# Performance work log

Hardware: AMD Instinct MI355X
Metric: run time of the kernel (lower is better)

## Reference

```python
import jax, jax.numpy as jnp
import numpy as np

B, S, E, H, A, D, V, L = 64, 196, 512, 512, 256, 512, 32000, 32
PAD_IDX = 2


def setup_inputs() -> dict:
    key = jax.random.key(0)
    ks = jax.random.split(key, 20)
    sc = 0.02
    return {
        "encoder_out": jax.random.normal(ks[0], (B, S, E), jnp.float32),
        "pooled": jax.random.normal(ks[1], (B, E), jnp.float32),
        "targets": jax.random.randint(ks[2], (B, L), 0, V, jnp.int64),
        "embedding": jax.random.normal(ks[3], (V, D), jnp.float32) * sc,
        "W_enc": jax.random.normal(ks[4], (A, E), jnp.float32) * sc,
        "b_enc": jnp.zeros((A,), jnp.float32),
        "W_dec": jax.random.normal(ks[5], (A, H), jnp.float32) * sc,
        "b_dec": jnp.zeros((A,), jnp.float32),
        "W_score": jax.random.normal(ks[6], (1, A), jnp.float32) * sc,
        "b_score": jnp.zeros((1,), jnp.float32),
        "W_ih": jax.random.normal(ks[7], (3 * H, D + E), jnp.float32) * sc,
        "W_hh": jax.random.normal(ks[8], (3 * H, H), jnp.float32) * sc,
        "b_ih": jnp.zeros((3 * H,), jnp.float32),
        "b_hh": jnp.zeros((3 * H,), jnp.float32),
        "W_out": jax.random.normal(ks[9], (V, H), jnp.float32) * sc,
        "b_out": jnp.zeros((V,), jnp.float32),
        "W_init": jax.random.normal(ks[10], (H, E), jnp.float32) * sc,
        "b_init": jnp.zeros((H,), jnp.float32),
    }


def reference(encoder_out, pooled, targets, embedding, W_enc, b_enc, W_dec,
              b_dec, W_score, b_score, W_ih, W_hh, b_ih, b_hh, W_out, b_out,
              W_init, b_init):
    # padding_idx=2: that embedding row is zero
    emb_tab = embedding.at[PAD_IDX].set(0.0)
    # initial hidden state from pooled features
    h0 = jnp.tanh(pooled @ W_init.T + b_init)              # (B, H)
    # encoder projection is step-invariant; hoist out of the loop
    enc_proj = jnp.einsum('bse,ae->bsa', encoder_out, W_enc) + b_enc  # (B,S,A)
    # teacher forcing (ratio=1.0): inputs are targets[:, :-1]
    tokens = targets[:, :-1].T                              # (L-1, B)

    def step(h, tok):
        embedded = emb_tab[tok]                             # (B, D)
        # Bahdanau attention
        dec_proj = h @ W_dec.T + b_dec                      # (B, A)
        energy = jnp.tanh(enc_proj + dec_proj[:, None, :])  # (B, S, A)
        scores = jnp.einsum('bsa,a->bs', energy, W_score[0]) + b_score[0]
        weights = jax.nn.softmax(scores, axis=1)            # (B, S)
        context = jnp.einsum('bs,bse->be', weights, encoder_out)  # (B, E)
        # GRU cell (PyTorch gate ordering: r, z, n)
        x = jnp.concatenate([embedded, context], axis=1)    # (B, D+E)
        gi = x @ W_ih.T + b_ih                              # (B, 3H)
        gh = h @ W_hh.T + b_hh                              # (B, 3H)
        gi_r, gi_z, gi_n = jnp.split(gi, 3, axis=1)
        gh_r, gh_z, gh_n = jnp.split(gh, 3, axis=1)
        r = jax.nn.sigmoid(gi_r + gh_r)
        z = jax.nn.sigmoid(gi_z + gh_z)
        n = jnp.tanh(gi_n + r * gh_n)
        h_new = (1.0 - z) * n + z * h
        logits = h_new @ W_out.T + b_out                    # (B, V)
        return h_new, logits

    _, logits = jax.lax.scan(step, h0, tokens)              # (L-1, B, V)
    return jnp.transpose(logits, (1, 0, 2))                 # (B, L-1, V)
```

## Files before the change

### kernel.cpp

```cpp
#include <hip/hip_runtime.h>

using bf16x8 = __attribute__((ext_vector_type(8))) short;
using f32x4  = __attribute__((ext_vector_type(4))) float;

__device__ inline float bf2f(unsigned short h){
  union { unsigned int u; float f; } v; v.u = ((unsigned int)h) << 16; return v.f;
}
__device__ inline unsigned short f2b(float x){
  union { float f; unsigned int u; } v; v.f = x;
  unsigned int r = (v.u + 0x7FFFu + ((v.u >> 16) & 1u)) >> 16;
  return (unsigned short)r;
}

__global__ void conv_k(const float* __restrict__ s, unsigned short* __restrict__ d, int n){
  int i = (blockIdx.x * 256 + threadIdx.x) * 4;
  if (i >= n) return;
  float4 v = *(const float4*)(s + i);
  unsigned int p0 = (unsigned int)f2b(v.x) | ((unsigned int)f2b(v.y) << 16);
  unsigned int p1 = (unsigned int)f2b(v.z) | ((unsigned int)f2b(v.w) << 16);
  *(uint2*)(d + i) = make_uint2(p0, p1);
}

__global__ void embed_k(const int* __restrict__ tgt, const float* __restrict__ emb,
                        unsigned short* __restrict__ out, int n){
  int idx = blockIdx.x * 256 + threadIdx.x;
  if (idx >= n) return;
  int d = idx & 511, m = idx >> 9, t = m >> 6, b = m & 63;
  int tok = tgt[b * 32 + t];
  float v = (tok == 2) ? 0.f : emb[(long)tok * 512 + d];
  out[idx] = f2b(v);
}

#define EPI_PLAIN 0
#define EPI_TANH  1
#define EPI_OUT   2

template<int EPI, bool AF32>
__global__ __launch_bounds__(256)
void gemm_bt(const void* __restrict__ Av, int lda,
             const unsigned short* __restrict__ Bp, int ldb,
             const float* __restrict__ bias,
             float* __restrict__ Cf, unsigned short* __restrict__ Cb, int ldc,
             int K,
             int n_split, const void* __restrict__ A2v,
             const unsigned short* __restrict__ B2p, int lda2, int ldb2)
{
  __shared__ __align__(16) unsigned short As[64][40];
  __shared__ __align__(16) unsigned short Bs[256][40];

  int m0 = blockIdx.x * 64;
  int n0 = blockIdx.y * 256;
  const void* Ap = Av; const unsigned short* Bq = Bp;
  int la = lda, lb = ldb, nB = n0;
  if (n_split > 0 && n0 >= n_split){ Ap = A2v; Bq = B2p; la = lda2; lb = ldb2; nB = n0 - n_split; }

  int tid  = threadIdx.x;
  int wave = tid >> 6, lane = tid & 63, quad = lane >> 4, lrow = lane & 15;

  f32x4 acc[4][4];
#pragma unroll
  for (int i = 0; i < 4; ++i)
#pragma unroll
    for (int j = 0; j < 4; ++j)
#pragma unroll
      for (int r = 0; r < 4; ++r) acc[i][j][r] = 0.f;

  int ar = tid >> 2, ac = (tid & 3) * 8;

  for (int k0 = 0; k0 < K; k0 += 32){
    if (AF32){
      const float* A32 = (const float*)Ap;
      const float4* src = (const float4*)(A32 + (long)(m0 + ar) * la + k0 + ac);
      float4 x0 = src[0], x1 = src[1];
      unsigned int p0 = (unsigned int)f2b(x0.x) | ((unsigned int)f2b(x0.y) << 16);
      unsigned int p1 = (unsigned int)f2b(x0.z) | ((unsigned int)f2b(x0.w) << 16);
      unsigned int p2 = (unsigned int)f2b(x1.x) | ((unsigned int)f2b(x1.y) << 16);
      unsigned int p3 = (unsigned int)f2b(x1.z) | ((unsigned int)f2b(x1.w) << 16);
      *(uint4*)&As[ar][ac] = make_uint4(p0, p1, p2, p3);
    } else {
      const unsigned short* A16 = (const unsigned short*)Ap;
      *(uint4*)&As[ar][ac] = *(const uint4*)(A16 + (long)(m0 + ar) * la + k0 + ac);
    }
#pragma unroll
    for (int c = 0; c < 4; ++c){
      int id = tid + c * 256; int br = id >> 2, bc = (id & 3) * 8;
      *(uint4*)&Bs[br][bc] = *(const uint4*)(Bq + (long)(nB + br) * lb + k0 + bc);
    }
    __syncthreads();

    bf16x8 af[4], bfr[4];
#pragma unroll
    for (int mf = 0; mf < 4; ++mf) af[mf]  = *(const bf16x8*)&As[mf * 16 + lrow][quad * 8];
#pragma unroll
    for (int nf = 0; nf < 4; ++nf) bfr[nf] = *(const bf16x8*)&Bs[wave * 64 + nf * 16 + lrow][quad * 8];
#pragma unroll
    for (int mf = 0; mf < 4; ++mf)
#pragma unroll
      for (int nf = 0; nf < 4; ++nf)
        acc[mf][nf] = __builtin_amdgcn_mfma_f32_16x16x32_bf16(af[mf], bfr[nf], acc[mf][nf], 0, 0, 0);
    __syncthreads();
  }

#pragma unroll
  for (int mf = 0; mf < 4; ++mf){
#pragma unroll
    for (int nf = 0; nf < 4; ++nf){
#pragma unroll
      for (int r = 0; r < 4; ++r){
        int m = m0 + mf * 16 + quad * 4 + r;
        int n = n0 + wave * 64 + nf * 16 + lrow;
        float v = acc[mf][nf][r];
        if (bias) v += bias[n];
        if (EPI == EPI_TANH){
          v = tanhf(v);
          Cf[(long)m * ldc + n] = v;
          Cb[(long)m * ldc + n] = f2b(v);
        } else if (EPI == EPI_OUT){
          Cf[(long)(m & 63) * (31 * 32000) + (long)(m >> 6) * 32000 + n] = v;
        } else {
          Cf[(long)m * ldc + n] = v;
        }
      }
    }
  }
}

__global__ __launch_bounds__(512)
void attn_step(const float* __restrict__ enc_proj,
               const float* __restrict__ enc_out,
               const float* __restrict__ W_score,
               const float* __restrict__ b_dec,
               const float* __restrict__ b_hh,
               const float* __restrict__ gi_emb,
               const float* __restrict__ giq,
               float* __restrict__ h_all,
               unsigned short* __restrict__ h_b16,
               const unsigned short* __restrict__ Wdec,
               unsigned short* __restrict__ ctx_b16,
               int t, int do_gates, int do_attn)
{
  int b = blockIdx.x, tid = threadIdx.x;
  __shared__ float sh_h[512];
  __shared__ float sdp[256];
  __shared__ float sbuf[512];
  __shared__ float sw[256];
  __shared__ float sred[512];
  __shared__ float swsc[256];

  float hv;
  if (do_gates){
    int j = tid;
    long ge = ((long)(t - 1) * 64 + b) * 1536;
    long gq = (long)b * 3072;
    float gir = gi_emb[ge + j]        + giq[gq + j];
    float giz = gi_emb[ge + 512 + j]  + giq[gq + 512 + j];
    float gin = gi_emb[ge + 1024 + j] + giq[gq + 1024 + j];
    float ghr = giq[gq + 1536 + j]        + b_hh[j];
    float ghz = giq[gq + 1536 + 512 + j]  + b_hh[512 + j];
    float ghn = giq[gq + 1536 + 1024 + j] + b_hh[1024 + j];
    float rr = 1.f / (1.f + __expf(-(gir + ghr)));
    float zz = 1.f / (1.f + __expf(-(giz + ghz)));
    float nn = tanhf(gin + rr * ghn);
    float hp = h_all[((long)(t - 1) * 64 + b) * 512 + j];
    hv = (1.f - zz) * nn + zz * hp;
    h_all[((long)t * 64 + b) * 512 + j] = hv;
    h_b16[((long)t * 64 + b) * 512 + j] = f2b(hv);
  } else {
    hv = h_all[((long)t * 64 + b) * 512 + tid];
  }
  sh_h[tid] = hv;
  if (tid < 256) swsc[tid] = W_score[tid];
  __syncthreads();
  if (!do_attn) return;

  {
    int a = tid & 255, half = tid >> 8;
    const uint4* wp = (const uint4*)(Wdec + a * 512 + half * 256);
    const float* hp = &sh_h[half * 256];
    float acc = 0.f;
#pragma unroll 8
    for (int c = 0; c < 32; ++c){
      uint4 wv = wp[c];
      acc += hp[c*8+0] * bf2f((unsigned short)(wv.x & 0xffff));
      acc += hp[c*8+1] * bf2f((unsigned short)(wv.x >> 16));
      acc += hp[c*8+2] * bf2f((unsigned short)(wv.y & 0xffff));
      acc += hp[c*8+3] * bf2f((unsigned short)(wv.y >> 16));
      acc += hp[c*8+4] * bf2f((unsigned short)(wv.z & 0xffff));
      acc += hp[c*8+5] * bf2f((unsigned short)(wv.z >> 16));
      acc += hp[c*8+6] * bf2f((unsigned short)(wv.w & 0xffff));
      acc += hp[c*8+7] * bf2f((unsigned short)(wv.w >> 16));
    }
    sbuf[tid] = acc;
    __syncthreads();
    if (tid < 256) sdp[tid] = sbuf[tid] + sbuf[tid + 256] + b_dec[tid];
    __syncthreads();
  }

  {
    int s = tid & 255, half = tid >> 8;
    float acc = 0.f;
    if (s < 196){
      const float* ep = enc_proj + ((long)b * 196 + s) * 256 + half * 128;
      const float* dp = &sdp[half * 128];
      const float* wv = &swsc[half * 128];
#pragma unroll 4
      for (int a = 0; a < 128; ++a){
        float x = ep[a] + dp[a];
        float e = __expf(2.f * x);
        acc += wv[a] * (1.f - 2.f / (e + 1.f));
      }
    }
    sbuf[tid] = acc;
    __syncthreads();
    float sc = (tid < 196) ? (sbuf[tid] + sbuf[tid + 256]) : -1e30f;
    sred[tid] = sc; __syncthreads();
    for (int off = 256; off > 0; off >>= 1){
      if (tid < off) sred[tid] = fmaxf(sred[tid], sred[tid + off]);
      __syncthreads();
    }
    float mx = sred[0]; __syncthreads();
    float e = (tid < 196) ? __expf(sc - mx) : 0.f;
    sred[tid] = e; __syncthreads();
    for (int off = 256; off > 0; off >>= 1){
      if (tid < off) sred[tid] += sred[tid + off];
      __syncthreads();
    }
    float inv = 1.f / sred[0];
    if (tid < 196) sw[tid] = e * inv;
    __syncthreads();
  }

  {
    const float* ep = enc_out + (long)b * 196 * 512 + tid;
    float acc = 0.f;
#pragma unroll 4
    for (int s = 0; s < 196; ++s) acc += sw[s] * ep[(long)s * 512];
    ctx_b16[b * 512 + tid] = f2b(acc);
  }
}

extern "C" void kernel_launch(void* const* d_in, const int* in_sizes, int n_in,
                              void* d_out, int out_size, void* d_ws, size_t ws_size,
                              hipStream_t stream)
{
  (void)in_sizes; (void)n_in; (void)out_size; (void)ws_size;
  const float* encoder_out = (const float*)d_in[0];
  const float* pooled      = (const float*)d_in[1];
  const int*   targets     = (const int*)d_in[2];
  const float* embedding   = (const float*)d_in[3];
  const float* W_enc  = (const float*)d_in[4];
  const float* b_enc  = (const float*)d_in[5];
  const float* W_dec  = (const float*)d_in[6];
  const float* b_dec  = (const float*)d_in[7];
  const float* W_score= (const float*)d_in[8];
  const float* W_ih   = (const float*)d_in[10];
  const float* W_hh   = (const float*)d_in[11];
  const float* b_ih   = (const float*)d_in[12];
  const float* b_hh   = (const float*)d_in[13];
  const float* W_out  = (const float*)d_in[14];
  const float* b_out  = (const float*)d_in[15];
  const float* W_init = (const float*)d_in[16];
  const float* b_init = (const float*)d_in[17];
  float* out = (float*)d_out;

  char* w = (char*)d_ws;
  float* enc_proj         = (float*)w;          w += 12845056;
  float* gi_emb           = (float*)w;          w += 12189696;
  float* h_all            = (float*)w;          w += 4194304;
  unsigned short* h_b16   = (unsigned short*)w; w += 2097152;
  float* giq              = (float*)w;          w += 786432;
  unsigned short* ctx_b16 = (unsigned short*)w; w += 65536;
  unsigned short* emb_b16 = (unsigned short*)w; w += 2031616;
  unsigned short* Wout_b  = (unsigned short*)w; w += 32768000;
  unsigned short* Wih_b   = (unsigned short*)w; w += 3145728;
  unsigned short* Whh_b   = (unsigned short*)w; w += 1572864;
  unsigned short* Wdec_b  = (unsigned short*)w; w += 262144;
  unsigned short* Winit_b = (unsigned short*)w; w += 524288;
  unsigned short* Wenc_b  = (unsigned short*)w; w += 262144;

  auto conv = [&](const float* s, unsigned short* d, int n){
    conv_k<<<dim3((n / 4 + 255) / 256), dim3(256), 0, stream>>>(s, d, n);
  };
  conv(W_out,  Wout_b,  32000 * 512);
  conv(W_ih,   Wih_b,   1536 * 1024);
  conv(W_hh,   Whh_b,   1536 * 512);
  conv(W_dec,  Wdec_b,  256 * 512);
  conv(W_init, Winit_b, 512 * 512);
  conv(W_enc,  Wenc_b,  256 * 512);
  embed_k<<<dim3((1984 * 512) / 256), dim3(256), 0, stream>>>(targets, embedding, emb_b16, 1984 * 512);

  gemm_bt<EPI_TANH, true><<<dim3(1, 2), 256, 0, stream>>>(
      pooled, 512, Winit_b, 512, b_init, h_all, h_b16, 512, 512, 0, nullptr, nullptr, 0, 0);
  gemm_bt<EPI_PLAIN, true><<<dim3(196, 1), 256, 0, stream>>>(
      encoder_out, 512, Wenc_b, 512, b_enc, enc_proj, nullptr, 256, 512, 0, nullptr, nullptr, 0, 0);
  gemm_bt<EPI_PLAIN, false><<<dim3(31, 6), 256, 0, stream>>>(
      emb_b16, 512, Wih_b, 1024, b_ih, gi_emb, nullptr, 1536, 512, 0, nullptr, nullptr, 0, 0);

  for (int t = 0; t < 31; ++t){
    attn_step<<<dim3(64), dim3(512), 0, stream>>>(
        enc_proj, encoder_out, W_score, b_dec, b_hh, gi_emb, giq,
        h_all, h_b16, Wdec_b, ctx_b16, t, (t > 0) ? 1 : 0, 1);
    gemm_bt<EPI_PLAIN, false><<<dim3(1, 12), 256, 0, stream>>>(
        ctx_b16, 512, Wih_b + 512, 1024, nullptr, giq, nullptr, 3072, 512,
        1536, h_b16 + (long)t * 64 * 512, Whh_b, 512, 512);
  }
  attn_step<<<dim3(64), dim3(512), 0, stream>>>(
      enc_proj, encoder_out, W_score, b_dec, b_hh, gi_emb, giq,
      h_all, h_b16, Wdec_b, ctx_b16, 31, 1, 0);

  gemm_bt<EPI_OUT, false><<<dim3(31, 125), 256, 0, stream>>>(
      h_b16 + 64 * 512, 512, Wout_b, 512, b_out, out, nullptr, 0, 512,
      0, nullptr, nullptr, 0, 0);
}
```

Before: 2.380 ms.

## Fuse whole recurrent decode loop into one persistent per-batch kernel

Replaces the 31-step loop of attention kernel plus gate GEMM launches with a single kernel. Each of 64 blocks (1024 threads) runs all timesteps for one batch row, keeping h, context and gate pre-activations in shared memory. It also stores enc_proj, gi_emb and encoder_out as bf16, uses packed bf16 dot2 instructions and fast tanh/sigmoid approximations, and adds a larger 128x256 tiled output GEMM. This removes about 60 launches and the global round trips for giq, but each step's gate matvec now streams 3 MB of weights per block from L2 with only 64 blocks active, and precision drops from the bf16 intermediates.

```diff
diff --git a/kernel.cpp b/kernel.cpp
--- a/kernel.cpp
+++ b/kernel.cpp
@@ -2,6 +2,19 @@
 
 using bf16x8 = __attribute__((ext_vector_type(8))) short;
 using f32x4  = __attribute__((ext_vector_type(4))) float;
+
+#if defined(__has_builtin)
+#  if __has_builtin(__builtin_amdgcn_fdot2_f32_bf16)
+#    define HAS_BF16_DOT 1
+#  endif
+#endif
+#ifndef HAS_BF16_DOT
+#  define HAS_BF16_DOT 0
+#endif
+
+#if HAS_BF16_DOT
+typedef __bf16 bf16x2v __attribute__((ext_vector_type(2)));
+#endif
 
 __device__ inline float bf2f(unsigned short h){
   union { unsigned int u; float f; } v; v.u = ((unsigned int)h) << 16; return v.f;
@@ -11,14 +24,36 @@
   unsigned int r = (v.u + 0x7FFFu + ((v.u >> 16) & 1u)) >> 16;
   return (unsigned short)r;
 }
+__device__ inline unsigned int pack2(float a, float b){
+  return (unsigned int)f2b(a) | ((unsigned int)f2b(b) << 16);
+}
+__device__ inline float bflo(unsigned int u){
+  union { unsigned int u; float f; } v; v.u = u << 16; return v.f;
+}
+__device__ inline float bfhi(unsigned int u){
+  union { unsigned int u; float f; } v; v.u = u & 0xffff0000u; return v.f;
+}
+__device__ inline float dot2p(unsigned int w, unsigned int x, float acc){
+#if HAS_BF16_DOT
+  return __builtin_amdgcn_fdot2_f32_bf16(
+      __builtin_bit_cast(bf16x2v, w), __builtin_bit_cast(bf16x2v, x), acc, false);
+#else
+  return fmaf(bfhi(w), bfhi(x), fmaf(bflo(w), bflo(x), acc));
+#endif
+}
+__device__ inline float tanh_fast(float x){
+  float e = __expf(2.f * x);
+  return 1.f - 2.f * __builtin_amdgcn_rcpf(e + 1.f);
+}
+__device__ inline float sigmoid_fast(float x){
+  return __builtin_amdgcn_rcpf(1.f + __expf(-x));
+}
 
 __global__ void conv_k(const float* __restrict__ s, unsigned short* __restrict__ d, int n){
   int i = (blockIdx.x * 256 + threadIdx.x) * 4;
   if (i >= n) return;
   float4 v = *(const float4*)(s + i);
-  unsigned int p0 = (unsigned int)f2b(v.x) | ((unsigned int)f2b(v.y) << 16);
-  unsigned int p1 = (unsigned int)f2b(v.z) | ((unsigned int)f2b(v.w) << 16);
-  *(uint2*)(d + i) = make_uint2(p0, p1);
+  *(uint2*)(d + i) = make_uint2(pack2(v.x, v.y), pack2(v.z, v.w));
 }
 
 __global__ void embed_k(const int* __restrict__ tgt, const float* __restrict__ emb,
@@ -31,9 +66,28 @@
   out[idx] = f2b(v);
 }
 
+__global__ void repack_wg(const float* __restrict__ Wih, const float* __restrict__ Whh,
+                          unsigned short* __restrict__ out){
+  int idx = (blockIdx.x * 256 + threadIdx.x) * 4;
+  if (idx >= 3072 * 512) return;
+  int j = idx >> 9, k = idx & 511;
+  const float* src = (j < 1536) ? (Wih + (long)j * 1024 + 512 + k)
+                                : (Whh + (long)(j - 1536) * 512 + k);
+  float4 v = *(const float4*)src;
+  *(uint2*)(out + idx) = make_uint2(pack2(v.x, v.y), pack2(v.z, v.w));
+}
+
+__global__ void repack_wih0(const float* __restrict__ Wih, unsigned short* __restrict__ out){
+  int idx = (blockIdx.x * 256 + threadIdx.x) * 4;
+  if (idx >= 1536 * 512) return;
+  int j = idx >> 9, k = idx & 511;
+  float4 v = *(const float4*)(Wih + (long)j * 1024 + k);
+  *(uint2*)(out + idx) = make_uint2(pack2(v.x, v.y), pack2(v.z, v.w));
+}
+
 #define EPI_PLAIN 0
 #define EPI_TANH  1
-#define EPI_OUT   2
+#define EPI_B16   3
 
 template<int EPI, bool AF32>
 __global__ __launch_bounds__(256)
@@ -41,20 +95,12 @@
              const unsigned short* __restrict__ Bp, int ldb,
              const float* __restrict__ bias,
              float* __restrict__ Cf, unsigned short* __restrict__ Cb, int ldc,
-             int K,
-             int n_split, const void* __restrict__ A2v,
-             const unsigned short* __restrict__ B2p, int lda2, int ldb2)
+             int K)
 {
   __shared__ __align__(16) unsigned short As[64][40];
   __shared__ __align__(16) unsigned short Bs[256][40];
-
-  int m0 = blockIdx.x * 64;
-  int n0 = blockIdx.y * 256;
-  const void* Ap = Av; const unsigned short* Bq = Bp;
-  int la = lda, lb = ldb, nB = n0;
-  if (n_split > 0 && n0 >= n_split){ Ap = A2v; Bq = B2p; la = lda2; lb = ldb2; nB = n0 - n_split; }
-
-  int tid  = threadIdx.x;
+  int m0 = blockIdx.x * 64, n0 = blockIdx.y * 256;
+  int tid = threadIdx.x;
   int wave = tid >> 6, lane = tid & 63, quad = lane >> 4, lrow = lane & 15;
 
   f32x4 acc[4][4];
@@ -69,25 +115,21 @@
 
   for (int k0 = 0; k0 < K; k0 += 32){
     if (AF32){
-      const float* A32 = (const float*)Ap;
-      const float4* src = (const float4*)(A32 + (long)(m0 + ar) * la + k0 + ac);
+      const float* A32 = (const float*)Av;
+      const float4* src = (const float4*)(A32 + (long)(m0 + ar) * lda + k0 + ac);
       float4 x0 = src[0], x1 = src[1];
-      unsigned int p0 = (unsigned int)f2b(x0.x) | ((unsigned int)f2b(x0.y) << 16);
-      unsigned int p1 = (unsigned int)f2b(x0.z) | ((unsigned int)f2b(x0.w) << 16);
-      unsigned int p2 = (unsigned int)f2b(x1.x) | ((unsigned int)f2b(x1.y) << 16);
-      unsigned int p3 = (unsigned int)f2b(x1.z) | ((unsigned int)f2b(x1.w) << 16);
-      *(uint4*)&As[ar][ac] = make_uint4(p0, p1, p2, p3);
+      *(uint4*)&As[ar][ac] = make_uint4(pack2(x0.x, x0.y), pack2(x0.z, x0.w),
+                                        pack2(x1.x, x1.y), pack2(x1.z, x1.w));
     } else {
-      const unsigned short* A16 = (const unsigned short*)Ap;
-      *(uint4*)&As[ar][ac] = *(const uint4*)(A16 + (long)(m0 + ar) * la + k0 + ac);
+      const unsigned short* A16 = (const unsigned short*)Av;
+      *(uint4*)&As[ar][ac] = *(const uint4*)(A16 + (long)(m0 + ar) * lda + k0 + ac);
     }
 #pragma unroll
     for (int c = 0; c < 4; ++c){
       int id = tid + c * 256; int br = id >> 2, bc = (id & 3) * 8;
-      *(uint4*)&Bs[br][bc] = *(const uint4*)(Bq + (long)(nB + br) * lb + k0 + bc);
-    }
-    __syncthreads();
-
+      *(uint4*)&Bs[br][bc] = *(const uint4*)(Bp + (long)(n0 + br) * ldb + k0 + bc);
+    }
+    __syncthreads();
     bf16x8 af[4], bfr[4];
 #pragma unroll
     for (int mf = 0; mf < 4; ++mf) af[mf]  = *(const bf16x8*)&As[mf * 16 + lrow][quad * 8];
@@ -102,140 +144,238 @@
   }
 
 #pragma unroll
-  for (int mf = 0; mf < 4; ++mf){
-#pragma unroll
-    for (int nf = 0; nf < 4; ++nf){
+  for (int mf = 0; mf < 4; ++mf)
+#pragma unroll
+    for (int nf = 0; nf < 4; ++nf)
 #pragma unroll
       for (int r = 0; r < 4; ++r){
         int m = m0 + mf * 16 + quad * 4 + r;
         int n = n0 + wave * 64 + nf * 16 + lrow;
-        float v = acc[mf][nf][r];
-        if (bias) v += bias[n];
+        float v = acc[mf][nf][r] + (bias ? bias[n] : 0.f);
         if (EPI == EPI_TANH){
           v = tanhf(v);
           Cf[(long)m * ldc + n] = v;
           Cb[(long)m * ldc + n] = f2b(v);
-        } else if (EPI == EPI_OUT){
-          Cf[(long)(m & 63) * (31 * 32000) + (long)(m >> 6) * 32000 + n] = v;
+        } else if (EPI == EPI_B16){
+          Cb[(long)m * ldc + n] = f2b(v);
         } else {
           Cf[(long)m * ldc + n] = v;
         }
       }
-    }
+}
+
+__global__ __launch_bounds__(256)
+void gemm_out(const unsigned short* __restrict__ A,
+              const unsigned short* __restrict__ B,
+              const float* __restrict__ bias,
+              float* __restrict__ out)
+{
+  __shared__ __align__(16) unsigned short As[128][40];
+  __shared__ __align__(16) unsigned short Bs[256][40];
+  int m0 = blockIdx.x * 128, n0 = blockIdx.y * 256;
+  int tid = threadIdx.x;
+  int wave = tid >> 6, lane = tid & 63, quad = lane >> 4, lrow = lane & 15;
+  int wm = wave >> 1, wn = wave & 1;
+
+  f32x4 acc[4][8];
+#pragma unroll
+  for (int i = 0; i < 4; ++i)
+#pragma unroll
+    for (int j = 0; j < 8; ++j)
+#pragma unroll
+      for (int r = 0; r < 4; ++r) acc[i][j][r] = 0.f;
+
+  int ar = tid >> 1, ac = (tid & 1) * 16;
+
+  for (int k0 = 0; k0 < 512; k0 += 32){
+    const unsigned short* as = A + (long)(m0 + ar) * 512 + k0 + ac;
+    *(uint4*)&As[ar][ac]     = *(const uint4*)(as);
+    *(uint4*)&As[ar][ac + 8] = *(const uint4*)(as + 8);
+#pragma unroll
+    for (int c = 0; c < 4; ++c){
+      int id = tid + c * 256; int br = id >> 2, bc = (id & 3) * 8;
+      *(uint4*)&Bs[br][bc] = *(const uint4*)(B + (long)(n0 + br) * 512 + k0 + bc);
+    }
+    __syncthreads();
+    bf16x8 af[4], bfr[8];
+#pragma unroll
+    for (int mf = 0; mf < 4; ++mf) af[mf]  = *(const bf16x8*)&As[wm * 64 + mf * 16 + lrow][quad * 8];
+#pragma unroll
+    for (int nf = 0; nf < 8; ++nf) bfr[nf] = *(const bf16x8*)&Bs[wn * 128 + nf * 16 + lrow][quad * 8];
+#pragma unroll
+    for (int mf = 0; mf < 4; ++mf)
+#pragma unroll
+      for (int nf = 0; nf < 8; ++nf)
+        acc[mf][nf] = __builtin_amdgcn_mfma_f32_16x16x32_bf16(af[mf], bfr[nf], acc[mf][nf], 0, 0, 0);
+    __syncthreads();
   }
-}
-
-__global__ __launch_bounds__(512)
-void attn_step(const float* __restrict__ enc_proj,
-               const float* __restrict__ enc_out,
-               const float* __restrict__ W_score,
-               const float* __restrict__ b_dec,
-               const float* __restrict__ b_hh,
-               const float* __restrict__ gi_emb,
-               const float* __restrict__ giq,
-               float* __restrict__ h_all,
-               unsigned short* __restrict__ h_b16,
-               const unsigned short* __restrict__ Wdec,
-               unsigned short* __restrict__ ctx_b16,
-               int t, int do_gates, int do_attn)
+
+#pragma unroll
+  for (int mf = 0; mf < 4; ++mf)
+#pragma unroll
+    for (int nf = 0; nf < 8; ++nf)
+#pragma unroll
+      for (int r = 0; r < 4; ++r){
+        int m = m0 + wm * 64 + mf * 16 + quad * 4 + r;
+        if (m < 1984){
+          int n = n0 + wn * 128 + nf * 16 + lrow;
+          out[(long)(m & 63) * 992000 + (long)(m >> 6) * 32000 + n] = acc[mf][nf][r] + bias[n];
+        }
+      }
+}
+
+__global__ __launch_bounds__(1024)
+void recur_k(const unsigned short* __restrict__ enc_proj16,
+             const unsigned short* __restrict__ enc_out16,
+             const float* __restrict__ W_score,
+             const float* __restrict__ b_dec,
+             const float* __restrict__ b_hh,
+             const unsigned short* __restrict__ gi_emb16,
+             const float* __restrict__ h0,
+             const unsigned short* __restrict__ Wdec16,
+             const unsigned short* __restrict__ Wg16,
+             unsigned short* __restrict__ h_b16)
 {
   int b = blockIdx.x, tid = threadIdx.x;
-  __shared__ float sh_h[512];
-  __shared__ float sdp[256];
-  __shared__ float sbuf[512];
-  __shared__ float sw[256];
-  __shared__ float sred[512];
-  __shared__ float swsc[256];
-
-  float hv;
-  if (do_gates){
-    int j = tid;
-    long ge = ((long)(t - 1) * 64 + b) * 1536;
-    long gq = (long)b * 3072;
-    float gir = gi_emb[ge + j]        + giq[gq + j];
-    float giz = gi_emb[ge + 512 + j]  + giq[gq + 512 + j];
-    float gin = gi_emb[ge + 1024 + j] + giq[gq + 1024 + j];
-    float ghr = giq[gq + 1536 + j]        + b_hh[j];
-    float ghz = giq[gq + 1536 + 512 + j]  + b_hh[512 + j];
-    float ghn = giq[gq + 1536 + 1024 + j] + b_hh[1024 + j];
-    float rr = 1.f / (1.f + __expf(-(gir + ghr)));
-    float zz = 1.f / (1.f + __expf(-(giz + ghz)));
-    float nn = tanhf(gin + rr * ghn);
-    float hp = h_all[((long)(t - 1) * 64 + b) * 512 + j];
-    hv = (1.f - zz) * nn + zz * hp;
-    h_all[((long)t * 64 + b) * 512 + j] = hv;
-    h_b16[((long)t * 64 + b) * 512 + j] = f2b(hv);
-  } else {
-    hv = h_all[((long)t * 64 + b) * 512 + tid];
-  }
-  sh_h[tid] = hv;
+  __shared__ __align__(16) float sh[512];
+  __shared__ __align__(16) float sdp[256];
+  __shared__ __align__(16) float sw[256];
+  __shared__ __align__(16) float sgq[3072];
+  __shared__ __align__(16) float sred[1024];
+  __shared__ __align__(16) float swred[16];
+  __shared__ __align__(16) float swsc[256];
+  __shared__ __align__(16) unsigned int shpk[256];
+  __shared__ __align__(16) unsigned int scpk[256];
+
+  if (tid < 512) sh[tid] = h0[b * 512 + tid];
   if (tid < 256) swsc[tid] = W_score[tid];
   __syncthreads();
-  if (!do_attn) return;
-
-  {
-    int a = tid & 255, half = tid >> 8;
-    const uint4* wp = (const uint4*)(Wdec + a * 512 + half * 256);
-    const float* hp = &sh_h[half * 256];
-    float acc = 0.f;
+  if (tid < 256) shpk[tid] = pack2(sh[2 * tid], sh[2 * tid + 1]);
+  __syncthreads();
+
+  for (int t = 0; t < 31; ++t){
+    {
+      int a = tid >> 2, q = tid & 3;
+      const unsigned short* wd = Wdec16 + a * 512 + q * 128;
+      float acc = 0.f;
 #pragma unroll 8
-    for (int c = 0; c < 32; ++c){
-      uint4 wv = wp[c];
-      acc += hp[c*8+0] * bf2f((unsigned short)(wv.x & 0xffff));
-      acc += hp[c*8+1] * bf2f((unsigned short)(wv.x >> 16));
-      acc += hp[c*8+2] * bf2f((unsigned short)(wv.y & 0xffff));
-      acc += hp[c*8+3] * bf2f((unsigned short)(wv.y >> 16));
-      acc += hp[c*8+4] * bf2f((unsigned short)(wv.z & 0xffff));
-      acc += hp[c*8+5] * bf2f((unsigned short)(wv.z >> 16));
-      acc += hp[c*8+6] * bf2f((unsigned short)(wv.w & 0xffff));
-      acc += hp[c*8+7] * bf2f((unsigned short)(wv.w >> 16));
-    }
-    sbuf[tid] = acc;
-    __syncthreads();
-    if (tid < 256) sdp[tid] = sbuf[tid] + sbuf[tid + 256] + b_dec[tid];
-    __syncthreads();
-  }
-
-  {
-    int s = tid & 255, half = tid >> 8;
-    float acc = 0.f;
-    if (s < 196){
-      const float* ep = enc_proj + ((long)b * 196 + s) * 256 + half * 128;
-      const float* dp = &sdp[half * 128];
-      const float* wv = &swsc[half * 128];
+      for (int i = 0; i < 16; ++i){
+        uint4 wv = *(const uint4*)(wd + i * 8);
+        uint4 hv = *(const uint4*)&shpk[q * 64 + i * 4];
+        acc = dot2p(wv.x, hv.x, acc);
+        acc = dot2p(wv.y, hv.y, acc);
+        acc = dot2p(wv.z, hv.z, acc);
+        acc = dot2p(wv.w, hv.w, acc);
+      }
+      acc += __shfl_xor(acc, 1);
+      acc += __shfl_xor(acc, 2);
+      if (q == 0) sdp[a] = acc + b_dec[a];
+    }
+    __syncthreads();
+
+    {
+      int s = tid & 255, q = tid >> 8;
+      float acc = 0.f;
+      if (s < 196){
+        const uint4* ep = (const uint4*)(enc_proj16 + ((b * 196 + s) << 8) + (q << 6));
+#pragma unroll
+        for (int i = 0; i < 8; ++i){
+          uint4 wv = ep[i];
+          int o = q * 64 + i * 8;
+          float4 d0 = *(const float4*)&sdp[o];
+          float4 d1 = *(const float4*)&sdp[o + 4];
+          float4 w0 = *(const float4*)&swsc[o];
+          float4 w1 = *(const float4*)&swsc[o + 4];
+          acc = fmaf(w0.x, tanh_fast(bflo(wv.x) + d0.x), acc);
+          acc = fmaf(w0.y, tanh_fast(bfhi(wv.x) + d0.y), acc);
+          acc = fmaf(w0.z, tanh_fast(bflo(wv.y) + d0.z), acc);
+          acc = fmaf(w0.w, tanh_fast(bfhi(wv.y) + d0.w), acc);
+          acc = fmaf(w1.x, tanh_fast(bflo(wv.z) + d1.x), acc);
+          acc = fmaf(w1.y, tanh_fast(bfhi(wv.z) + d1.y), acc);
+          acc = fmaf(w1.z, tanh_fast(bflo(wv.w) + d1.z), acc);
+          acc = fmaf(w1.w, tanh_fast(bfhi(wv.w) + d1.w), acc);
+        }
+      }
+      sred[tid] = acc;
+      __syncthreads();
+      float sc = -1e30f;
+      if (tid < 196) sc = sred[tid] + sred[tid + 256] + sred[tid + 512] + sred[tid + 768];
+      float mx = sc;
+#pragma unroll
+      for (int o = 32; o >= 1; o >>= 1) mx = fmaxf(mx, __shfl_xor(mx, o));
+      if (tid < 256 && (tid & 63) == 0) swred[tid >> 6] = mx;
+      __syncthreads();
+      mx = fmaxf(fmaxf(swred[0], swred[1]), fmaxf(swred[2], swred[3]));
+      float ev = (tid < 196) ? __expf(sc - mx) : 0.f;
+      float sm = ev;
+#pragma unroll
+      for (int o = 32; o >= 1; o >>= 1) sm += __shfl_xor(sm, o);
+      if (tid < 256 && (tid & 63) == 0) swred[8 + (tid >> 6)] = sm;
+      __syncthreads();
+      float inv = __builtin_amdgcn_rcpf(swred[8] + swred[9] + swred[10] + swred[11]);
+      if (tid < 196) sw[tid] = ev * inv;
+    }
+    __syncthreads();
+
+    {
+      int e = tid & 511, q = tid >> 9;
+      const unsigned short* ebase = enc_out16 + ((b * 196 + q * 98) << 9) + e;
+      float acc = 0.f;
+#pragma unroll 7
+      for (int i = 0; i < 98; ++i)
+        acc = fmaf(sw[q * 98 + i], bf2f(ebase[i * 512]), acc);
+      sred[tid] = acc;
+      __syncthreads();
+      if (tid < 512) sred[tid] = sred[tid] + sred[tid + 512];
+      __syncthreads();
+      if (tid < 256) scpk[tid] = pack2(sred[2 * tid], sred[2 * tid + 1]);
+    }
+    __syncthreads();
+
+    {
+      const unsigned short* w0 = Wg16 + (long)tid * 512;
+      const unsigned short* w1 = w0 + 1024 * 512;
+      const unsigned short* w2 = w0 + 2048 * 512;
+      bool mid_ctx = (tid < 512);
+      float a0 = 0.f, a1 = 0.f, a2 = 0.f;
 #pragma unroll 4
-      for (int a = 0; a < 128; ++a){
-        float x = ep[a] + dp[a];
-        float e = __expf(2.f * x);
-        acc += wv[a] * (1.f - 2.f / (e + 1.f));
+      for (int i = 0; i < 64; ++i){
+        uint4 x0 = *(const uint4*)(w0 + i * 8);
+        uint4 x1 = *(const uint4*)(w1 + i * 8);
+        uint4 x2 = *(const uint4*)(w2 + i * 8);
+        uint4 oc = *(const uint4*)&scpk[i * 4];
+        uint4 oh = *(const uint4*)&shpk[i * 4];
+        uint4 om = mid_ctx ? oc : oh;
+        a0 = dot2p(x0.x, oc.x, a0); a0 = dot2p(x0.y, oc.y, a0);
+        a0 = dot2p(x0.z, oc.z, a0); a0 = dot2p(x0.w, oc.w, a0);
+        a1 = dot2p(x1.x, om.x, a1); a1 = dot2p(x1.y, om.y, a1);
+        a1 = dot2p(x1.z, om.z, a1); a1 = dot2p(x1.w, om.w, a1);
+        a2 = dot2p(x2.x, oh.x, a2); a2 = dot2p(x2.y, oh.y, a2);
+        a2 = dot2p(x2.z, oh.z, a2); a2 = dot2p(x2.w, oh.w, a2);
       }
-    }
-    sbuf[tid] = acc;
-    __syncthreads();
-    float sc = (tid < 196) ? (sbuf[tid] + sbuf[tid + 256]) : -1e30f;
-    sred[tid] = sc; __syncthreads();
-    for (int off = 256; off > 0; off >>= 1){
-      if (tid < off) sred[tid] = fmaxf(sred[tid], sred[tid + off]);
-      __syncthreads();
-    }
-    float mx = sred[0]; __syncthreads();
-    float e = (tid < 196) ? __expf(sc - mx) : 0.f;
-    sred[tid] = e; __syncthreads();
-    for (int off = 256; off > 0; off >>= 1){
-      if (tid < off) sred[tid] += sred[tid + off];
-      __syncthreads();
-    }
-    float inv = 1.f / sred[0];
-    if (tid < 196) sw[tid] = e * inv;
-    __syncthreads();
-  }
-
-  {
-    const float* ep = enc_out + (long)b * 196 * 512 + tid;
-    float acc = 0.f;
-#pragma unroll 4
-    for (int s = 0; s < 196; ++s) acc += sw[s] * ep[(long)s * 512];
-    ctx_b16[b * 512 + tid] = f2b(acc);
+      sgq[tid] = a0; sgq[tid + 1024] = a1; sgq[tid + 2048] = a2;
+    }
+    __syncthreads();
+
+    if (tid < 512){
+      int j = tid;
+      const unsigned short* ge = gi_emb16 + (long)(t * 64 + b) * 1536;
+      float gir = bf2f(ge[j])        + sgq[j];
+      float giz = bf2f(ge[j + 512])  + sgq[j + 512];
+      float gin = bf2f(ge[j + 1024]) + sgq[j + 1024];
+      float ghr = sgq[1536 + j] + b_hh[j];
+      float ghz = sgq[2048 + j] + b_hh[512 + j];
+      float ghn = sgq[2560 + j] + b_hh[1024 + j];
+      float r = sigmoid_fast(gir + ghr);
+      float z = sigmoid_fast(giz + ghz);
+      float n = tanh_fast(gin + r * ghn);
+      float hn = (1.f - z) * n + z * sh[j];
+      sh[j] = hn;
+      h_b16[(long)((t + 1) * 64 + b) * 512 + j] = f2b(hn);
+    }
+    __syncthreads();
+    if (tid < 256) shpk[tid] = pack2(sh[2 * tid], sh[2 * tid + 1]);
+    __syncthreads();
   }
 }
 
@@ -264,51 +404,42 @@
   float* out = (float*)d_out;
 
   char* w = (char*)d_ws;
-  float* enc_proj         = (float*)w;          w += 12845056;
-  float* gi_emb           = (float*)w;          w += 12189696;
-  float* h_all            = (float*)w;          w += 4194304;
-  unsigned short* h_b16   = (unsigned short*)w; w += 2097152;
-  float* giq              = (float*)w;          w += 786432;
-  unsigned short* ctx_b16 = (unsigned short*)w; w += 65536;
-  unsigned short* emb_b16 = (unsigned short*)w; w += 2031616;
-  unsigned short* Wout_b  = (unsigned short*)w; w += 32768000;
-  unsigned short* Wih_b   = (unsigned short*)w; w += 3145728;
-  unsigned short* Whh_b   = (unsigned short*)w; w += 1572864;
-  unsigned short* Wdec_b  = (unsigned short*)w; w += 262144;
-  unsigned short* Winit_b = (unsigned short*)w; w += 524288;
-  unsigned short* Wenc_b  = (unsigned short*)w; w += 262144;
+  unsigned short* enc_proj16 = (unsigned short*)w; w += 6422528;
+  unsigned short* gi_emb16   = (unsigned short*)w; w += 6094848;
+  float* h0f                 = (float*)w;          w += 131072;
+  unsigned short* h_b16      = (unsigned short*)w; w += 2162688;
+  unsigned short* emb_b16    = (unsigned short*)w; w += 2031616;
+  unsigned short* enc_out16  = (unsigned short*)w; w += 12845056;
+  unsigned short* Wout_b     = (unsigned short*)w; w += 32768000;
+  unsigned short* Wihe_b     = (unsigned short*)w; w += 1572864;
+  unsigned short* Wdec_b     = (unsigned short*)w; w += 262144;
+  unsigned short* Winit_b    = (unsigned short*)w; w += 524288;
+  unsigned short* Wenc_b     = (unsigned short*)w; w += 262144;
+  unsigned short* Wg_b       = (unsigned short*)w; w += 3145728;
 
   auto conv = [&](const float* s, unsigned short* d, int n){
     conv_k<<<dim3((n / 4 + 255) / 256), dim3(256), 0, stream>>>(s, d, n);
   };
   conv(W_out,  Wout_b,  32000 * 512);
-  conv(W_ih,   Wih_b,   1536 * 1024);
-  conv(W_hh,   Whh_b,   1536 * 512);
   conv(W_dec,  Wdec_b,  256 * 512);
   conv(W_init, Winit_b, 512 * 512);
   conv(W_enc,  Wenc_b,  256 * 512);
+  conv(encoder_out, enc_out16, 64 * 196 * 512);
   embed_k<<<dim3((1984 * 512) / 256), dim3(256), 0, stream>>>(targets, embedding, emb_b16, 1984 * 512);
+  repack_wg<<<dim3(3072 * 512 / 4 / 256), dim3(256), 0, stream>>>(W_ih, W_hh, Wg_b);
+  repack_wih0<<<dim3(1536 * 512 / 4 / 256), dim3(256), 0, stream>>>(W_ih, Wihe_b);
 
   gemm_bt<EPI_TANH, true><<<dim3(1, 2), 256, 0, stream>>>(
-      pooled, 512, Winit_b, 512, b_init, h_all, h_b16, 512, 512, 0, nullptr, nullptr, 0, 0);
-  gemm_bt<EPI_PLAIN, true><<<dim3(196, 1), 256, 0, stream>>>(
-      encoder_out, 512, Wenc_b, 512, b_enc, enc_proj, nullptr, 256, 512, 0, nullptr, nullptr, 0, 0);
-  gemm_bt<EPI_PLAIN, false><<<dim3(31, 6), 256, 0, stream>>>(
-      emb_b16, 512, Wih_b, 1024, b_ih, gi_emb, nullptr, 1536, 512, 0, nullptr, nullptr, 0, 0);
-
-  for (int t = 0; t < 31; ++t){
-    attn_step<<<dim3(64), dim3(512), 0, stream>>>(
-        enc_proj, encoder_out, W_score, b_dec, b_hh, gi_emb, giq,
-        h_all, h_b16, Wdec_b, ctx_b16, t, (t > 0) ? 1 : 0, 1);
-    gemm_bt<EPI_PLAIN, false><<<dim3(1, 12), 256, 0, stream>>>(
-        ctx_b16, 512, Wih_b + 512, 1024, nullptr, giq, nullptr, 3072, 512,
-        1536, h_b16 + (long)t * 64 * 512, Whh_b, 512, 512);
-  }
-  attn_step<<<dim3(64), dim3(512), 0, stream>>>(
-      enc_proj, encoder_out, W_score, b_dec, b_hh, gi_emb, giq,
-      h_all, h_b16, Wdec_b, ctx_b16, 31, 1, 0);
-
-  gemm_bt<EPI_OUT, false><<<dim3(31, 125), 256, 0, stream>>>(
-      h_b16 + 64 * 512, 512, Wout_b, 512, b_out, out, nullptr, 0, 512,
-      0, nullptr, nullptr, 0, 0);
-}
+      pooled, 512, Winit_b, 512, b_init, h0f, h_b16, 512, 512);
+  gemm_bt<EPI_B16, true><<<dim3(196, 1), 256, 0, stream>>>(
+      encoder_out, 512, Wenc_b, 512, b_enc, nullptr, enc_proj16, 256, 512);
+  gemm_bt<EPI_B16, false><<<dim3(31, 6), 256, 0, stream>>>(
+      emb_b16, 512, Wihe_b, 512, b_ih, nullptr, gi_emb16, 1536, 512);
+
+  recur_k<<<dim3(64), dim3(1024), 0, stream>>>(
+      enc_proj16, enc_out16, W_score, b_dec, b_hh, gi_emb16, h0f,
+      Wdec_b, Wg_b, h_b16);
+
+  gemm_out<<<dim3(16, 125), 256, 0, stream>>>(
+      h_b16 + 64 * 512, Wout_b, b_out, out);
+}
```

After: 4.523 ms. 1.9x slower.
